# Optimization experiments

Measured on AMD Instinct MI355X. Metric: run time of the kernel, lower is better.

The kernel has to match this reference:

```python
import jax, jax.numpy as jnp
import numpy as np

NEG = -1e10  # the original uses -10000000000.0
B, T, L = 64, 512, 64
START, END = 0, L - 1


def setup_inputs() -> dict:
    key = jax.random.key(0)
    k_em, k_tr, k_len = jax.random.split(key, 3)
    emission_scores = jax.random.normal(k_em, (B, T, L), dtype=jnp.float32)
    # transition initialized as in __init__: randn with start column / end row masked
    transition = jax.random.normal(k_tr, (L, L), dtype=jnp.float32)
    transition = transition.at[:, START].set(NEG)
    transition = transition.at[END, :].set(NEG)
    sent_lens = jax.random.randint(k_len, (B,), T // 2, T + 1, dtype=jnp.int32)
    return {"emission_scores": emission_scores, "transition": transition,
            "sent_lens": sent_lens}


def reference(emission_scores, transition, sent_lens):
    # --- calculate_all_scores ---
    em = emission_scores.at[:, :, START].set(NEG).at[:, :, END].set(NEG)
    # scores[b,t,y_prev,y_t] = transition[y_prev,y_t] + emission[b,t,y_t]
    scores = transition[None, None, :, :] + em[:, :, None, :]  # [B,T,L,L]
    scores = scores.at[:, 1:, START, :].set(NEG)

    # --- forward_score: sequential DP via scan ---
    alpha0 = scores[:, 0, START, :]  # [B,L]

    def step(alpha_prev, s_t):  # s_t: [B,L,L]
        alpha_t = jax.nn.logsumexp(alpha_prev[:, :, None] + s_t, axis=1)
        return alpha_t, alpha_t

    _, alphas_rest = jax.lax.scan(step, alpha0, jnp.moveaxis(scores[:, 1:], 1, 0))
    alpha = jnp.concatenate([alpha0[:, None, :], jnp.moveaxis(alphas_rest, 0, 1)],
                            axis=1)  # [B,T,L]

    idx = (sent_lens - 1).astype(jnp.int32)[:, None, None]  # [B,1,1]
    last_alpha = jnp.take_along_axis(alpha, idx, axis=1)[:, 0, :]  # [B,L]
    last_alpha = last_alpha + transition[:, END][None, :]
    log_Z = jax.nn.logsumexp(last_alpha, axis=1)  # [B]
    return alpha, log_Z
```

## Files before the change

kernel.cpp:

```cpp
#include <hip/hip_runtime.h>

#define NEGV -10000000000.0f
constexpr int Bn = 64, Tn = 512, Ln = 64;
constexpr int CK = 32;
constexpr int NC = 16;
constexpr int QP = 68;

typedef float f32x16 __attribute__((ext_vector_type(16)));
typedef __bf16 bf16x8 __attribute__((ext_vector_type(8)));
typedef unsigned int u32;
typedef unsigned short u16;

__device__ inline float waveMaxF(float v) {
#pragma unroll
    for (int off = 32; off > 0; off >>= 1)
        v = fmaxf(v, __shfl_xor(v, off, 64));
    return v;
}
__device__ inline u32 packbf(float a, float b) {
    u32 ua = __float_as_uint(a) + 0x8000u;
    u32 ub = __float_as_uint(b) + 0x8000u;
    return (ua >> 16) | (ub & 0xffff0000u);
}
__device__ inline float lo16f(u32 d) { return __uint_as_float(d << 16); }
__device__ inline float hi16f(u32 d) { return __uint_as_float(d & 0xffff0000u); }

template <bool FIRST>
__device__ void chunk_scan(const float* __restrict__ emb,
                           float* __restrict__ outb, float* uLDS,
                           const float* Ecol, float entry, int t0, int j, int len,
                           float trSj, float* aLastOut, float* aFinalOut) {
    const bool edge = (j == 0) || (j == Ln - 1);
    float emq[4];
#pragma unroll
    for (int tt = 0; tt < 4; ++tt) {
        float v = emb[(t0 + tt) * Ln + j];
        emq[tt] = edge ? NEGV : v;
    }
    float aPrev, mPrev, u;
    int tauStart;
    if (FIRST) {
        float a0 = trSj + emq[0];
        outb[t0 * Ln + j] = a0;
        aPrev = a0;
        mPrev = __shfl(a0, 1, 64);
        u = __expf(a0 - mPrev);
        tauStart = 1;
    } else {
        aPrev = entry;
        mPrev = __shfl(entry, 1, 64);
        u = __expf(entry - mPrev);
        tauStart = 0;
    }
    float aLast = *aLastOut;
#pragma unroll 4
    for (int tau = tauStart; tau < CK; ++tau) {
        const int t = t0 + tau;
        uLDS[j] = u;
        const float em_t = emq[tau & 3];
        const int tp = tau + 4;
        if (tp < CK) {
            float v = emb[(t0 + tp) * Ln + j];
            emq[tp & 3] = edge ? NEGV : v;
        }
        float mNext = __shfl(aPrev, 1, 64);
        float cf = __expf(em_t + (mPrev - mNext));
        float acc0 = 0.f, acc1 = 0.f, acc2 = 0.f, acc3 = 0.f;
        const float4* u4 = reinterpret_cast<const float4*>(uLDS);
#pragma unroll
        for (int i4 = 0; i4 < 16; ++i4) {
            float4 uv = u4[i4];
            acc0 = fmaf(uv.x, Ecol[4 * i4 + 0], acc0);
            acc1 = fmaf(uv.y, Ecol[4 * i4 + 1], acc1);
            acc2 = fmaf(uv.z, Ecol[4 * i4 + 2], acc2);
            acc3 = fmaf(uv.w, Ecol[4 * i4 + 3], acc3);
        }
        float S = (acc0 + acc1) + (acc2 + acc3);
        float lg = __logf(S);
        lg = (S > 0.f) ? lg : NEGV;
        float a_t = em_t + (mPrev + lg);
        outb[t * Ln + j] = a_t;
        if (t == len - 1) aLast = a_t;
        u = S * cf;
        aPrev = a_t;
        mPrev = mNext;
    }
    *aLastOut = aLast;
    *aFinalOut = aPrev;
}

__global__ __launch_bounds__(128) void crf_passA(const float* __restrict__ em,
                                                 const float* __restrict__ tr,
                                                 float* __restrict__ out,
                                                 float* __restrict__ wsE,
                                                 float* __restrict__ wsS) {
    const int b = blockIdx.x & 63;
    const int cix = blockIdx.x >> 6;
    const int J = threadIdx.x >> 6;
    const int L = threadIdx.x & 63;
    __shared__ alignas(16) float gtab[CK * 64];
    __shared__ alignas(16) u16 Qlds[64 * QP];
    __shared__ alignas(16) float uLDS[64];
    __shared__ float sLDS[2];
    __shared__ float sigLDS[2];

    if (cix == 0) {
        if (J == 1) return;
        float Ecol[Ln];
#pragma unroll
        for (int i = 0; i < Ln; ++i) Ecol[i] = __expf(tr[i * Ln + L]);
        const float trSj = tr[L];
        const float* emb = em + (size_t)b * Tn * Ln;
        float* outb = out + (size_t)b * Tn * Ln;
        float dummyLast = 0.f, aFinal;
        chunk_scan<true>(emb, outb, uLDS, Ecol, 0.f, 0, L,  -1, trSj, &dummyLast, &aFinal);
        wsE[b * 1024 + 1 * 64 + L] = aFinal;
        return;
    }

    const int t0 = CK * cix;
    const int c31 = L & 31;
    const int h = L >> 5;

    {
        float orig[16], sv[16];
        const int tb = t0 + 16 * J;
#pragma unroll
        for (int r = 0; r < 16; ++r) {
            float v = em[((size_t)b * Tn + (tb + r)) * Ln + L];
            if (L == 0 || L == Ln - 1) v = NEGV;
            orig[r] = v;
            sv[r] = v;
        }
#pragma unroll
        for (int off = 32; off > 0; off >>= 1) {
#pragma unroll
            for (int r = 0; r < 16; ++r)
                sv[r] = fmaxf(sv[r], __shfl_xor(sv[r], off, 64));
        }
        float ssum = 0.f;
#pragma unroll
        for (int r = 0; r < 16; ++r) {
            gtab[(16 * J + r) * 64 + L] = __expf(orig[r] - sv[r]);
            ssum += sv[r];
        }
        if (L == 0) sLDS[J] = ssum;
    }
    __syncthreads();
    const float sSum = sLDS[0] + sLDS[1];

    uint4 Ap[2][4];
#pragma unroll
    for (int I = 0; I < 2; ++I)
#pragma unroll
        for (int kc = 0; kc < 4; ++kc) {
            float e[8];
#pragma unroll
            for (int q = 0; q < 8; ++q) {
                int k = 16 * kc + 8 * h + q;
                e[q] = __expf(tr[k * Ln + 32 * I + c31]);
            }
            Ap[I][kc] = make_uint4(packbf(e[0], e[1]), packbf(e[2], e[3]),
                                   packbf(e[4], e[5]), packbf(e[6], e[7]));
        }

    const int n = 32 * J + c31;
    {
        const float* trn = tr + n * Ln + 32 * h;
        const float* g0 = gtab + 32 * h;
#pragma unroll
        for (int k4 = 0; k4 < 8; ++k4) {
            float v0 = __expf(trn[4 * k4 + 0]) * g0[4 * k4 + 0];
            float v1 = __expf(trn[4 * k4 + 1]) * g0[4 * k4 + 1];
            float v2 = __expf(trn[4 * k4 + 2]) * g0[4 * k4 + 2];
            float v3 = __expf(trn[4 * k4 + 3]) * g0[4 * k4 + 3];
            uint2 w;
            w.x = packbf(v0, v1);
            w.y = packbf(v2, v3);
            *(uint2*)&Qlds[n * QP + 32 * h + 4 * k4] = w;
        }
    }

    float sig_w = 0.f;
    float wm = 1.0f;
    const f32x16 Z = (f32x16)(0.0f);
    for (int tau = 1; tau < CK; ++tau) {
        uint4 Bp[4];
#pragma unroll
        for (int kc = 0; kc < 4; ++kc) {
            const u16* p = &Qlds[n * QP + 16 * kc + 8 * h];
            uint2 q0 = *(const uint2*)(p);
            uint2 q1 = *(const uint2*)(p + 4);
            Bp[kc] = make_uint4(q0.x, q0.y, q1.x, q1.y);
        }
        f32x16 acc0 = Z, acc1 = Z;
#pragma unroll
        for (int kc = 0; kc < 4; ++kc) {
            acc0 = __builtin_amdgcn_mfma_f32_32x32x16_bf16(
                __builtin_bit_cast(bf16x8, Ap[0][kc]),
                __builtin_bit_cast(bf16x8, Bp[kc]), acc0, 0, 0, 0);
            acc1 = __builtin_amdgcn_mfma_f32_32x32x16_bf16(
                __builtin_bit_cast(bf16x8, Ap[1][kc]),
                __builtin_bit_cast(bf16x8, Bp[kc]), acc1, 0, 0, 0);
        }
        const bool doRescale = ((tau & 3) == 0);
        const bool doMeasure = ((tau & 3) == 2);
        float rr = 1.0f;
        if (doRescale) {
            rr = 1.0f / wm;
            sig_w += __logf(wm);
        }
        float lmax = 0.f;
#pragma unroll
        for (int I = 0; I < 2; ++I) {
#pragma unroll
            for (int rg = 0; rg < 4; ++rg) {
                const int k0 = 32 * I + 8 * rg + 4 * h;
                float4 G = *(const float4*)&gtab[tau * 64 + k0];
                float v0 = (I ? acc1 : acc0)[4 * rg + 0] * (G.x * rr);
                float v1 = (I ? acc1 : acc0)[4 * rg + 1] * (G.y * rr);
                float v2 = (I ? acc1 : acc0)[4 * rg + 2] * (G.z * rr);
                float v3 = (I ? acc1 : acc0)[4 * rg + 3] * (G.w * rr);
                if (doMeasure) lmax = fmaxf(lmax, fmaxf(fmaxf(v0, v1), fmaxf(v2, v3)));
                uint2 w;
                w.x = packbf(v0, v1);
                w.y = packbf(v2, v3);
                *(uint2*)&Qlds[n * QP + k0] = w;
            }
        }
        if (doMeasure) wm = waveMaxF(lmax);
    }

    if (L == 0) sigLDS[J] = sSum + sig_w;
    __syncthreads();
    const float sg0 = sigLDS[0], sg1 = sigLDS[1];
    const float smax = fmaxf(sg0, sg1);
    const float fh = __expf((h ? sg1 : sg0) - smax);
    const int r = 32 * J + c31;
    float rv[32];
    float lmaxr = 0.f;
#pragma unroll
    for (int i = 0; i < 32; ++i) {
        float v = __uint_as_float(((u32)Qlds[(32 * h + i) * QP + r]) << 16) * fh;
        rv[i] = v;
        lmaxr = fmaxf(lmaxr, v);
    }
    float rmax = fmaxf(lmaxr, __shfl_xor(lmaxr, 32, 64));
    float inv = (rmax > 0.f) ? 1.0f / rmax : 0.f;
    float sj = (rmax > 0.f) ? smax + __logf(rmax) : 0.f;
    u32* og = (u32*)out + (size_t)b * (Tn * Ln) + (size_t)cix * (CK * Ln) + r * 32 + h * 16;
#pragma unroll
    for (int w8 = 0; w8 < 4; ++w8) {
        uint4 w;
        w.x = packbf(rv[8 * w8 + 0] * inv, rv[8 * w8 + 1] * inv);
        w.y = packbf(rv[8 * w8 + 2] * inv, rv[8 * w8 + 3] * inv);
        w.z = packbf(rv[8 * w8 + 4] * inv, rv[8 * w8 + 5] * inv);
        w.w = packbf(rv[8 * w8 + 6] * inv, rv[8 * w8 + 7] * inv);
        *(uint4*)(og + 4 * w8) = w;
    }
    if (h == 0) wsS[b * 1024 + cix * 64 + r] = sj;
}

__global__ __launch_bounds__(64) void crf_passB(const float* __restrict__ out,
                                                float* __restrict__ wsE,
                                                const float* __restrict__ wsS) {
    const int b = blockIdx.x;
    const int j = threadIdx.x;
    __shared__ alignas(16) float uL[64];
    const u32* Qbase = (const u32*)out + (size_t)b * (Tn * Ln);

    float e = wsE[b * 1024 + 1 * 64 + j];
    uint4 nxt[8];
    float signxt = wsS[b * 1024 + 1 * 64 + j];
#pragma unroll
    for (int r = 0; r < 8; ++r) nxt[r] = *(const uint4*)(Qbase + 1 * (CK * Ln) + j * 32 + 4 * r);

#pragma unroll
    for (int c = 1; c <= 14; ++c) {
        uint4 cur[8];
#pragma unroll
        for (int r = 0; r < 8; ++r) cur[r] = nxt[r];
        float sig = signxt;
        if (c < 14) {
#pragma unroll
            for (int r = 0; r < 8; ++r)
                nxt[r] = *(const uint4*)(Qbase + (size_t)(c + 1) * (CK * Ln) + j * 32 + 4 * r);
            signxt = wsS[b * 1024 + (c + 1) * 64 + j];
        }
        float m = __shfl(e, 1, 64);
        uL[j] = __expf(e - m);
        const float4* u4 = reinterpret_cast<const float4*>(uL);
        float S = 0.f;
#pragma unroll
        for (int i4 = 0; i4 < 16; ++i4) {
            float4 uv = u4[i4];
            u32 d0 = ((const u32*)cur)[2 * i4];
            u32 d1 = ((const u32*)cur)[2 * i4 + 1];
            S = fmaf(uv.x, lo16f(d0), S);
            S = fmaf(uv.y, hi16f(d0), S);
            S = fmaf(uv.z, lo16f(d1), S);
            S = fmaf(uv.w, hi16f(d1), S);
        }
        float a;
        if (S > 0.f) a = m + sig + __logf(S);
        else a = m + NEGV + ((j == 0) ? NEGV : 0.f);
        e = a;
        wsE[b * 1024 + (c + 1) * 64 + j] = e;
    }
}

__global__ __launch_bounds__(64) void crf_passC(const float* __restrict__ em,
                                                const float* __restrict__ tr,
                                                const int* __restrict__ lens,
                                                float* __restrict__ out,
                                                const float* __restrict__ wsE) {
    const int b = blockIdx.x & 63;
    const int cix = 1 + (blockIdx.x >> 6);
    const int j = threadIdx.x;
    __shared__ alignas(16) float uLDS[64];

    float Ecol[Ln];
#pragma unroll
    for (int i = 0; i < Ln; ++i) Ecol[i] = __expf(tr[i * Ln + j]);
    const float trEj = tr[j * Ln + (Ln - 1)];
    const int len = lens[b];
    const float* emb = em + (size_t)b * Tn * Ln;
    float* outb = out + (size_t)b * Tn * Ln;
    const float entry = wsE[b * 1024 + cix * 64 + j];

    float aLast = 0.f, aFinal;
    chunk_scan<false>(emb, outb, uLDS, Ecol, entry, CK * cix, j, len, 0.f, &aLast, &aFinal);

    if (((len - 1) >> 5) == cix) {
        float last = aLast + trEj;
        float m2 = last;
#pragma unroll
        for (int off = 32; off > 0; off >>= 1)
            m2 = fmaxf(m2, __shfl_xor(m2, off, 64));
        float e2 = __expf(last - m2);
#pragma unroll
        for (int off = 32; off > 0; off >>= 1)
            e2 += __shfl_xor(e2, off, 64);
        if (j == 0) out[(size_t)Bn * Tn * Ln + b] = m2 + __logf(e2);
    }
}

__global__ __launch_bounds__(64) void crf_fallback(const float* __restrict__ em,
                                                   const float* __restrict__ tr,
                                                   const int* __restrict__ lens,
                                                   float* __restrict__ out) {
    const int b = blockIdx.x;
    const int j = threadIdx.x;
    __shared__ alignas(16) float uLDS[Ln];
    float E[Ln];
#pragma unroll
    for (int i = 0; i < Ln; ++i) E[i] = __expf(tr[i * Ln + j]);
    const float trSj = tr[j];
    const float trEj = tr[j * Ln + (Ln - 1)];
    const int len = lens[b];
    const bool edge = (j == 0) || (j == Ln - 1);
    const float* emb = em + (size_t)b * Tn * Ln;
    float* outb = out + (size_t)b * Tn * Ln;
    float emq[4];
#pragma unroll
    for (int tt = 0; tt < 4; ++tt) {
        float v = emb[tt * Ln + j];
        emq[tt] = edge ? NEGV : v;
    }
    float a = trSj + emq[0];
    outb[j] = a;
    float aPrev = a, aLast = a;
    float mPrev = __shfl(a, 1, 64);
    float u = __expf(a - mPrev);
#pragma unroll 4
    for (int t = 1; t < Tn; ++t) {
        uLDS[j] = u;
        const float em_t = emq[t & 3];
        const int tp = t + 4;
        if (tp < Tn) {
            float v = emb[tp * Ln + j];
            emq[tp & 3] = edge ? NEGV : v;
        }
        float mNext = __shfl(aPrev, 1, 64);
        float cf = __expf(em_t + (mPrev - mNext));
        float acc0 = 0.f, acc1 = 0.f, acc2 = 0.f, acc3 = 0.f;
        const float4* u4 = reinterpret_cast<const float4*>(uLDS);
#pragma unroll
        for (int i4 = 0; i4 < 16; ++i4) {
            float4 uv = u4[i4];
            acc0 = fmaf(uv.x, E[4 * i4 + 0], acc0);
            acc1 = fmaf(uv.y, E[4 * i4 + 1], acc1);
            acc2 = fmaf(uv.z, E[4 * i4 + 2], acc2);
            acc3 = fmaf(uv.w, E[4 * i4 + 3], acc3);
        }
        float S = (acc0 + acc1) + (acc2 + acc3);
        float lg = __logf(S);
        lg = (S > 0.f) ? lg : NEGV;
        float a_t = em_t + (mPrev + lg);
        outb[t * Ln + j] = a_t;
        if (t == len - 1) aLast = a_t;
        u = S * cf;
        aPrev = a_t;
        mPrev = mNext;
    }
    float last = aLast + trEj;
    float m2 = last;
#pragma unroll
    for (int off = 32; off > 0; off >>= 1)
        m2 = fmaxf(m2, __shfl_xor(m2, off, 64));
    float e2 = __expf(last - m2);
#pragma unroll
    for (int off = 32; off > 0; off >>= 1)
        e2 += __shfl_xor(e2, off, 64);
    if (j == 0) out[(size_t)Bn * Tn * Ln + b] = m2 + __logf(e2);
}

extern "C" void kernel_launch(void* const* d_in, const int* in_sizes, int n_in,
                              void* d_out, int out_size, void* d_ws, size_t ws_size,
                              hipStream_t stream) {
    const float* em = (const float*)d_in[0];
    const float* tr = (const float*)d_in[1];
    const int* lens = (const int*)d_in[2];
    float* out = (float*)d_out;
    const size_t wsNeed = 2u * 64 * 16 * 64 * sizeof(float);
    if (ws_size >= wsNeed) {
        float* wsE = (float*)d_ws;
        float* wsS = wsE + 64 * 16 * 64;
        crf_passA<<<dim3(1024), dim3(128), 0, stream>>>(em, tr, out, wsE, wsS);
        crf_passB<<<dim3(64), dim3(64), 0, stream>>>(out, wsE, wsS);
        crf_passC<<<dim3(960), dim3(64), 0, stream>>>(em, tr, lens, out, wsE);
    } else {
        crf_fallback<<<dim3(Bn), dim3(64), 0, stream>>>(em, tr, lens, out);
    }
}
```

Measured before the change: 134.8 us.

## Batch pass C chunk scan across sequences with bf16 MFMA and add logZ kernel

Pass C used to run one 64-thread block per (sequence, chunk), each doing a scalar per-label logsumexp recurrence. It now runs one 128-thread block per chunk that covers all 64 sequences. Each step's transition is done as a bf16 MFMA matmul in the exp domain, with periodic max rescaling, and alpha is written out through log2. Pass A's Q recurrence also moves from an LDS round trip to registers, swapping halves with cross-lane shuffles. A separate small kernel now computes log_Z. The risks are only 15 blocks occupying the GPU and bf16 precision loss in the pass C recurrence.

After: 194.8 us. +44.6%, slower.

```diff
diff --git a/kernel.cpp b/kernel.cpp
--- a/kernel.cpp
+++ b/kernel.cpp
@@ -3,8 +3,9 @@
 #define NEGV -10000000000.0f
 constexpr int Bn = 64, Tn = 512, Ln = 64;
 constexpr int CK = 32;
-constexpr int NC = 16;
 constexpr int QP = 68;
+constexpr float L2E = 1.4426950408889634f;
+constexpr float LN2 = 0.6931471805599453f;
 
 typedef float f32x16 __attribute__((ext_vector_type(16)));
 typedef __bf16 bf16x8 __attribute__((ext_vector_type(8)));
@@ -24,6 +25,8 @@
 }
 __device__ inline float lo16f(u32 d) { return __uint_as_float(d << 16); }
 __device__ inline float hi16f(u32 d) { return __uint_as_float(d & 0xffff0000u); }
+__device__ inline float fexp2(float x) { return __builtin_amdgcn_exp2f(x); }
+__device__ inline float flog2(float x) { return __builtin_amdgcn_logf(x); }
 
 template <bool FIRST>
 __device__ void chunk_scan(const float* __restrict__ emb,
@@ -165,21 +168,18 @@
         }
 
     const int n = 32 * J + c31;
-    {
-        const float* trn = tr + n * Ln + 32 * h;
-        const float* g0 = gtab + 32 * h;
-#pragma unroll
-        for (int k4 = 0; k4 < 8; ++k4) {
-            float v0 = __expf(trn[4 * k4 + 0]) * g0[4 * k4 + 0];
-            float v1 = __expf(trn[4 * k4 + 1]) * g0[4 * k4 + 1];
-            float v2 = __expf(trn[4 * k4 + 2]) * g0[4 * k4 + 2];
-            float v3 = __expf(trn[4 * k4 + 3]) * g0[4 * k4 + 3];
-            uint2 w;
-            w.x = packbf(v0, v1);
-            w.y = packbf(v2, v3);
-            *(uint2*)&Qlds[n * QP + 32 * h + 4 * k4] = w;
-        }
-    }
+    uint2 P[2][4];
+#pragma unroll
+    for (int I = 0; I < 2; ++I)
+#pragma unroll
+        for (int rg = 0; rg < 4; ++rg) {
+            const int k0 = 32 * I + 8 * rg + 4 * h;
+            float4 tv = *(const float4*)&tr[n * Ln + k0];
+            float4 gv = *(const float4*)&gtab[k0];
+            float v0 = __expf(tv.x) * gv.x, v1 = __expf(tv.y) * gv.y;
+            float v2 = __expf(tv.z) * gv.z, v3 = __expf(tv.w) * gv.w;
+            P[I][rg] = make_uint2(packbf(v0, v1), packbf(v2, v3));
+        }
 
     float sig_w = 0.f;
     float wm = 1.0f;
@@ -188,10 +188,14 @@
         uint4 Bp[4];
 #pragma unroll
         for (int kc = 0; kc < 4; ++kc) {
-            const u16* p = &Qlds[n * QP + 16 * kc + 8 * h];
-            uint2 q0 = *(const uint2*)(p);
-            uint2 q1 = *(const uint2*)(p + 4);
-            Bp[kc] = make_uint4(q0.x, q0.y, q1.x, q1.y);
+            const int I = kc >> 1;
+            uint2 keep = P[I][2 * (kc & 1) + h];
+            uint2 send = P[I][2 * (kc & 1) + (1 - h)];
+            uint2 recv;
+            recv.x = (u32)__shfl_xor((int)send.x, 32, 64);
+            recv.y = (u32)__shfl_xor((int)send.y, 32, 64);
+            Bp[kc] = (h == 0) ? make_uint4(keep.x, keep.y, recv.x, recv.y)
+                              : make_uint4(recv.x, recv.y, keep.x, keep.y);
         }
         f32x16 acc0 = Z, acc1 = Z;
 #pragma unroll
@@ -212,7 +216,7 @@
         }
         float lmax = 0.f;
 #pragma unroll
-        for (int I = 0; I < 2; ++I) {
+        for (int I = 0; I < 2; ++I)
 #pragma unroll
             for (int rg = 0; rg < 4; ++rg) {
                 const int k0 = 32 * I + 8 * rg + 4 * h;
@@ -222,15 +226,18 @@
                 float v2 = (I ? acc1 : acc0)[4 * rg + 2] * (G.z * rr);
                 float v3 = (I ? acc1 : acc0)[4 * rg + 3] * (G.w * rr);
                 if (doMeasure) lmax = fmaxf(lmax, fmaxf(fmaxf(v0, v1), fmaxf(v2, v3)));
-                uint2 w;
-                w.x = packbf(v0, v1);
-                w.y = packbf(v2, v3);
-                *(uint2*)&Qlds[n * QP + k0] = w;
+                P[I][rg] = make_uint2(packbf(v0, v1), packbf(v2, v3));
             }
-        }
         if (doMeasure) wm = waveMaxF(lmax);
     }
 
+#pragma unroll
+    for (int I = 0; I < 2; ++I)
+#pragma unroll
+        for (int rg = 0; rg < 4; ++rg) {
+            const int k0 = 32 * I + 8 * rg + 4 * h;
+            *(uint2*)&Qlds[n * QP + k0] = P[I][rg];
+        }
     if (L == 0) sigLDS[J] = sSum + sig_w;
     __syncthreads();
     const float sg0 = sigLDS[0], sg1 = sigLDS[1];
@@ -309,40 +316,158 @@
     }
 }
 
-__global__ __launch_bounds__(64) void crf_passC(const float* __restrict__ em,
-                                                const float* __restrict__ tr,
-                                                const int* __restrict__ lens,
-                                                float* __restrict__ out,
-                                                const float* __restrict__ wsE) {
-    const int b = blockIdx.x & 63;
-    const int cix = 1 + (blockIdx.x >> 6);
+__global__ __launch_bounds__(128) void crf_passC(const float* __restrict__ em,
+                                                 const float* __restrict__ tr,
+                                                 float* __restrict__ out,
+                                                 const float* __restrict__ wsE) {
+    const int cix = 1 + blockIdx.x;
+    const int J = threadIdx.x >> 6;
+    const int L = threadIdx.x & 63;
+    const int h = L >> 5, c31 = L & 31;
+    const int b = 32 * J + c31;
+    const int t0 = CK * cix;
+
+    uint4 Ap[2][4];
+#pragma unroll
+    for (int I = 0; I < 2; ++I)
+#pragma unroll
+        for (int kc = 0; kc < 4; ++kc) {
+            float e[8];
+#pragma unroll
+            for (int q = 0; q < 8; ++q) {
+                int k = 16 * kc + 8 * h + q;
+                e[q] = __expf(tr[k * Ln + 32 * I + c31]);
+            }
+            Ap[I][kc] = make_uint4(packbf(e[0], e[1]), packbf(e[2], e[3]),
+                                   packbf(e[4], e[5]), packbf(e[6], e[7]));
+        }
+
+    const float* we = wsE + b * 1024 + cix * 64;
+    float sig;
+    uint2 P[2][4];
+    {
+        float4 av[2][4];
+        float mx = -3e38f;
+#pragma unroll
+        for (int I = 0; I < 2; ++I)
+#pragma unroll
+            for (int rg = 0; rg < 4; ++rg) {
+                const int k0 = 32 * I + 8 * rg + 4 * h;
+                float4 a4 = *(const float4*)&we[k0];
+                av[I][rg] = a4;
+                mx = fmaxf(mx, fmaxf(fmaxf(a4.x, a4.y), fmaxf(a4.z, a4.w)));
+            }
+        mx = fmaxf(mx, __shfl_xor(mx, 32, 64));
+        sig = mx;
+#pragma unroll
+        for (int I = 0; I < 2; ++I)
+#pragma unroll
+            for (int rg = 0; rg < 4; ++rg) {
+                float4 a4 = av[I][rg];
+                float v0 = fexp2((a4.x - sig) * L2E), v1 = fexp2((a4.y - sig) * L2E);
+                float v2 = fexp2((a4.z - sig) * L2E), v3 = fexp2((a4.w - sig) * L2E);
+                P[I][rg] = make_uint2(packbf(v0, v1), packbf(v2, v3));
+            }
+    }
+
+    const float* pe = em + ((size_t)b * Tn + t0) * Ln;
+    float* po = out + ((size_t)b * Tn + t0) * Ln;
+
+    float4 e0[2][4];
+#pragma unroll
+    for (int I = 0; I < 2; ++I)
+#pragma unroll
+        for (int rg = 0; rg < 4; ++rg)
+            e0[I][rg] = *(const float4*)&pe[32 * I + 8 * rg + 4 * h];
+
+    float wmUse = 1.0f;
+    const f32x16 Z = (f32x16)(0.0f);
+    for (int tau = 0; tau < CK; ++tau) {
+        const bool even = ((tau & 1) == 0);
+        float rr = 1.0f, dsig = 0.0f;
+        if (even && tau >= 2) {
+            rr = 1.0f / wmUse;
+            dsig = LN2 * flog2(wmUse);
+        }
+        uint4 Bp[4];
+#pragma unroll
+        for (int kc = 0; kc < 4; ++kc) {
+            const int I = kc >> 1;
+            uint2 keep = P[I][2 * (kc & 1) + h];
+            uint2 send = P[I][2 * (kc & 1) + (1 - h)];
+            uint2 recv;
+            recv.x = (u32)__shfl_xor((int)send.x, 32, 64);
+            recv.y = (u32)__shfl_xor((int)send.y, 32, 64);
+            Bp[kc] = (h == 0) ? make_uint4(keep.x, keep.y, recv.x, recv.y)
+                              : make_uint4(recv.x, recv.y, keep.x, keep.y);
+        }
+        f32x16 acc0 = Z, acc1 = Z;
+#pragma unroll
+        for (int kc = 0; kc < 4; ++kc) {
+            acc0 = __builtin_amdgcn_mfma_f32_32x32x16_bf16(
+                __builtin_bit_cast(bf16x8, Ap[0][kc]),
+                __builtin_bit_cast(bf16x8, Bp[kc]), acc0, 0, 0, 0);
+            acc1 = __builtin_amdgcn_mfma_f32_32x32x16_bf16(
+                __builtin_bit_cast(bf16x8, Ap[1][kc]),
+                __builtin_bit_cast(bf16x8, Bp[kc]), acc1, 0, 0, 0);
+        }
+        float4 e1[2][4];
+        if (tau + 1 < CK) {
+#pragma unroll
+            for (int I = 0; I < 2; ++I)
+#pragma unroll
+                for (int rg = 0; rg < 4; ++rg)
+                    e1[I][rg] = *(const float4*)&pe[(tau + 1) * Ln + 32 * I + 8 * rg + 4 * h];
+        }
+        float lmax = 0.f;
+#pragma unroll
+        for (int I = 0; I < 2; ++I)
+#pragma unroll
+            for (int rg = 0; rg < 4; ++rg) {
+                const int k0 = 32 * I + 8 * rg + 4 * h;
+                float4 ev = e0[I][rg];
+                if (k0 == 0) ev.x = NEGV;
+                if (k0 == 60) ev.w = NEGV;
+                float c0 = (I ? acc1 : acc0)[4 * rg + 0];
+                float c1 = (I ? acc1 : acc0)[4 * rg + 1];
+                float c2 = (I ? acc1 : acc0)[4 * rg + 2];
+                float c3 = (I ? acc1 : acc0)[4 * rg + 3];
+                float4 al;
+                al.x = ev.x + ((c0 > 0.f) ? LN2 * flog2(c0) + sig : NEGV);
+                al.y = ev.y + ((c1 > 0.f) ? LN2 * flog2(c1) + sig : NEGV);
+                al.z = ev.z + ((c2 > 0.f) ? LN2 * flog2(c2) + sig : NEGV);
+                al.w = ev.w + ((c3 > 0.f) ? LN2 * flog2(c3) + sig : NEGV);
+                *(float4*)&po[tau * Ln + k0] = al;
+                float v0 = c0 * (fexp2(ev.x * L2E) * rr);
+                float v1 = c1 * (fexp2(ev.y * L2E) * rr);
+                float v2 = c2 * (fexp2(ev.z * L2E) * rr);
+                float v3 = c3 * (fexp2(ev.w * L2E) * rr);
+                if (even) lmax = fmaxf(lmax, fmaxf(fmaxf(v0, v1), fmaxf(v2, v3)));
+                P[I][rg] = make_uint2(packbf(v0, v1), packbf(v2, v3));
+            }
+        if (even) wmUse = fmaxf(lmax, __shfl_xor(lmax, 32, 64));
+        sig += dsig;
+        if (tau + 1 < CK) {
+#pragma unroll
+            for (int I = 0; I < 2; ++I)
+#pragma unroll
+                for (int rg = 0; rg < 4; ++rg) e0[I][rg] = e1[I][rg];
+        }
+    }
+}
+
+__global__ __launch_bounds__(64) void crf_logZ(const float* __restrict__ tr,
+                                               const int* __restrict__ lens,
+                                               float* __restrict__ out) {
+    const int b = blockIdx.x;
     const int j = threadIdx.x;
-    __shared__ alignas(16) float uLDS[64];
-
-    float Ecol[Ln];
-#pragma unroll
-    for (int i = 0; i < Ln; ++i) Ecol[i] = __expf(tr[i * Ln + j]);
-    const float trEj = tr[j * Ln + (Ln - 1)];
-    const int len = lens[b];
-    const float* emb = em + (size_t)b * Tn * Ln;
-    float* outb = out + (size_t)b * Tn * Ln;
-    const float entry = wsE[b * 1024 + cix * 64 + j];
-
-    float aLast = 0.f, aFinal;
-    chunk_scan<false>(emb, outb, uLDS, Ecol, entry, CK * cix, j, len, 0.f, &aLast, &aFinal);
-
-    if (((len - 1) >> 5) == cix) {
-        float last = aLast + trEj;
-        float m2 = last;
-#pragma unroll
-        for (int off = 32; off > 0; off >>= 1)
-            m2 = fmaxf(m2, __shfl_xor(m2, off, 64));
-        float e2 = __expf(last - m2);
-#pragma unroll
-        for (int off = 32; off > 0; off >>= 1)
-            e2 += __shfl_xor(e2, off, 64);
-        if (j == 0) out[(size_t)Bn * Tn * Ln + b] = m2 + __logf(e2);
-    }
+    float a = out[(size_t)b * Tn * Ln + (size_t)(lens[b] - 1) * Ln + j] + tr[j * Ln + (Ln - 1)];
+    float m2 = waveMaxF(a);
+    float e2 = __expf(a - m2);
+#pragma unroll
+    for (int off = 32; off > 0; off >>= 1)
+        e2 += __shfl_xor(e2, off, 64);
+    if (j == 0) out[(size_t)Bn * Tn * Ln + b] = m2 + __logf(e2);
 }
 
 __global__ __launch_bounds__(64) void crf_fallback(const float* __restrict__ em,
@@ -428,7 +553,8 @@
         float* wsS = wsE + 64 * 16 * 64;
         crf_passA<<<dim3(1024), dim3(128), 0, stream>>>(em, tr, out, wsE, wsS);
         crf_passB<<<dim3(64), dim3(64), 0, stream>>>(out, wsE, wsS);
-        crf_passC<<<dim3(960), dim3(64), 0, stream>>>(em, tr, lens, out, wsE);
+        crf_passC<<<dim3(15), dim3(128), 0, stream>>>(em, tr, out, wsE);
+        crf_logZ<<<dim3(64), dim3(64), 0, stream>>>(tr, lens, out);
     } else {
         crf_fallback<<<dim3(Bn), dim3(64), 0, stream>>>(em, tr, lens, out);
     }
```
